# Performance work log

Measured on AMD Instinct MI355X. Metric: run time of the kernel, lower is better.

Reference implementation:

```python
import jax, jax.numpy as jnp
import numpy as np

N_NODE = 40000
EMB = 100
LAYERS = 2
B = 512
L = 50
N = 50
E = 800000


def _l2norm(x, axis=-1, eps=1e-12):
    n = jnp.sqrt(jnp.sum(x * x, axis=axis, keepdims=True))
    return x / jnp.maximum(n, eps)


def _item_conv(rows, cols, vals, emb, b):
    # sparse A @ X repeated LAYERS times, stack, l2-normalize rows, weighted sum
    finals = [emb]
    x = emb
    for _ in range(LAYERS):
        x = jax.ops.segment_sum(vals[:, None] * x[cols], rows, num_segments=emb.shape[0])
        finals.append(x)
    f = _l2norm(jnp.stack(finals, 0))                      # [LAYERS+1, n, d]
    return jnp.sum(b[:, None, None] * f, axis=0)


def _session_conv(adj_dense, emb, a):
    finals = [emb]
    x = emb
    for _ in range(LAYERS):
        x = adj_dense @ x
        finals.append(x)
    f = _l2norm(jnp.stack(finals, 0))
    return jnp.sum(a[:, None, None] * f, axis=0)


def _gat(h, adj, a0, a1, a2, a3):
    # e_k[b,i,j] = leakyrelu(sum_d h[b,i,d]*h[b,j,d]*a_k[d]); never materialize [B,N,N,D]
    def score(a):
        return jax.nn.leaky_relu(jnp.einsum('bid,bjd->bij', h * a[:, 0], h), 0.2)
    e0, e1, e2, e3 = score(a0), score(a1), score(a2), score(a3)
    neg = jnp.float32(-9e15)
    alpha = jnp.where(adj == 1, e0, neg)
    alpha = jnp.where(adj == 2, e1, alpha)
    alpha = jnp.where(adj == 3, e2, alpha)
    alpha = jnp.where(adj == 4, e3, alpha)
    alpha = jax.nn.softmax(alpha, axis=-1)
    return jnp.einsum('bij,bjd->bid', alpha, h)


def _get_seq(emb_table, rev, h, alias, mix=0.8):
    seq_h = emb_table[rev]                                  # [B,L,D]
    bidx = jnp.arange(rev.shape[0])[:, None]
    seq_h_ = h[bidx, alias]                                 # [B,L,D]
    return (1.0 - mix) * seq_h + mix * seq_h_               # eval: dropout = identity


def _soft_attention(seq_h, mask_f, session_len, pos_emb, w1_W, w1_b, glu1_W, glu1_b, glu2_W, w2):
    hs = jnp.sum(seq_h, axis=1) / session_len               # [B,D]
    pos = jnp.broadcast_to(pos_emb[:seq_h.shape[1]][None], seq_h.shape)
    nh = jnp.tanh(jnp.concatenate([pos, seq_h], -1) @ w1_W.T + w1_b)
    nh = jax.nn.sigmoid(nh @ glu1_W.T + glu1_b + (hs @ glu2_W.T)[:, None, :])
    beta = (nh @ w2) * mask_f[..., None]                    # [B,L,1]
    return jnp.sum(beta * seq_h, axis=1)                    # [B,D]


def setup_inputs() -> dict:
    key = jax.random.key(0)
    ks = jax.random.split(key, 30)
    stdv = 1.0 / np.sqrt(EMB)
    u = lambda k, s: jax.random.uniform(k, s, jnp.float32, -stdv, stdv)
    return {
        'tar': jax.random.randint(ks[0], (B,), 0, N_NODE),
        'reversed_sess_item': jax.random.randint(ks[1], (B, L), 0, N_NODE + 1),
        'mask': jnp.ones((B, L), jnp.int32),
        'session_len': jnp.ones((B, 1), jnp.float32),
        'session_adj': jax.random.uniform(ks[2], (B, B), jnp.float32),
        'is_train': 0,
        'items': jax.random.randint(ks[3], (B, N), 0, N_NODE + 1),
        'adj': jax.random.randint(ks[4], (B, N, N), 0, 5),
        'alias_session': jax.random.randint(ks[5], (B, L), 0, N),
        'gnn_rows': jax.random.randint(ks[6], (E,), 0, N_NODE),
        'gnn_cols': jax.random.randint(ks[7], (E,), 0, N_NODE),
        'gnn_vals': jax.random.uniform(ks[8], (E,), jnp.float32),
        'nodes_emb': u(ks[9], (N_NODE, EMB)),
        'b_item': jnp.ones((LAYERS + 1,), jnp.float32),
        'a_sess': jnp.ones((LAYERS + 1,), jnp.float32),
        'a0': u(ks[10], (EMB, 1)), 'a1': u(ks[11], (EMB, 1)),
        'a2': u(ks[12], (EMB, 1)), 'a3': u(ks[13], (EMB, 1)),
        'w1_W': u(ks[14], (EMB, 2 * EMB)), 'w1_b': u(ks[15], (EMB,)),
        'w2': u(ks[16], (EMB, 1)),
        'glu1_W': u(ks[17], (EMB, EMB)), 'glu1_b': u(ks[18], (EMB,)),
        'glu2_W': u(ks[19], (EMB, EMB)),
        'pos_emb': u(ks[20], (150, EMB)),
    }


def reference(tar, reversed_sess_item, mask, session_len, session_adj, is_train,
              items, adj, alias_session, gnn_rows, gnn_cols, gnn_vals,
              nodes_emb, b_item, a_sess, a0, a1, a2, a3,
              w1_W, w1_b, w2, glu1_W, glu1_b, glu2_W, pos_emb):
    mask_f = mask.astype(jnp.float32)
    zeros = jnp.zeros((1, EMB), jnp.float32)
    emb_gnn = _item_conv(gnn_rows, gnn_cols, gnn_vals, nodes_emb, b_item)
    # eval mode: both dropouts are identity
    e1t = jnp.concatenate([zeros, emb_gnn], 0)
    e2t = jnp.concatenate([zeros, emb_gnn], 0)
    embeddings = e1t + e2t

    h1 = _gat(e1t[items], adj, a0, a1, a2, a3)
    h1 = _get_seq(e1t, reversed_sess_item, h1, alias_session, 0.8)
    h2 = _gat(e2t[items], adj, a0, a1, a2, a3)
    h2 = _get_seq(e2t, reversed_sess_item, h2, alias_session, 0.8)

    sel1 = _soft_attention(h1, mask_f, session_len, pos_emb, w1_W, w1_b, glu1_W, glu1_b, glu2_W, w2)
    sel1 = _session_conv(session_adj, sel1, a_sess)
    sel2 = _soft_attention(h2, mask_f, session_len, pos_emb, w1_W, w1_b, glu1_W, glu1_b, glu2_W, w2)
    sel2 = _session_conv(session_adj, sel2, a_sess)

    con_loss = jnp.float32(0.0)  # is_train == 0 (inference path)

    seq_h = sel1 + sel2
    scores = seq_h @ embeddings[1:].T                       # [B, N_NODE]
    logp = jax.nn.log_softmax(scores + 1e-8, axis=-1)
    loss = -jnp.mean(logp[jnp.arange(scores.shape[0]), tar])
    return (con_loss, loss, scores)
```

## Files before the change

### kernel.cpp

```cpp
#include <hip/hip_runtime.h>
#include <hip/hip_bf16.h>
#include <math.h>

#define N_NODE 40000
#define EMB 100
#define BB 512
#define LL 50
#define NI 50
#define EDG 800000
#define SCAN_BLOCKS 157

typedef short s16x8 __attribute__((ext_vector_type(8)));
typedef float f32x4 __attribute__((ext_vector_type(4)));

__global__ void khist(const int* __restrict__ rows, int* __restrict__ counts) {
  int e = blockIdx.x * 256 + threadIdx.x;
  atomicAdd(&counts[rows[e]], 1);
}

__global__ __launch_bounds__(256) void kscan1(const int* __restrict__ counts,
                                              int* __restrict__ scanout,
                                              int* __restrict__ blocksums, int n) {
  __shared__ int wsum[4];
  int tid = threadIdx.x;
  int i = blockIdx.x * 256 + tid;
  int v = (i < n) ? counts[i] : 0;
  int x = v;
  #pragma unroll
  for (int off = 1; off < 64; off <<= 1) {
    int t = __shfl_up(x, off, 64);
    if ((tid & 63) >= off) x += t;
  }
  int w = tid >> 6, lane = tid & 63;
  if (lane == 63) wsum[w] = x;
  __syncthreads();
  int woff = 0;
  #pragma unroll
  for (int k = 0; k < 4; ++k) woff += (k < w) ? wsum[k] : 0;
  int incl = x + woff;
  if (i < n) scanout[i] = incl - v;
  if (tid == 255) blocksums[blockIdx.x] = incl;
}

__global__ __launch_bounds__(256) void kscan2(int* __restrict__ blocksums, int nb) {
  __shared__ int wsum[4];
  int tid = threadIdx.x;
  int v = (tid < nb) ? blocksums[tid] : 0;
  int x = v;
  #pragma unroll
  for (int off = 1; off < 64; off <<= 1) {
    int t = __shfl_up(x, off, 64);
    if ((tid & 63) >= off) x += t;
  }
  int w = tid >> 6, lane = tid & 63;
  if (lane == 63) wsum[w] = x;
  __syncthreads();
  int woff = 0;
  #pragma unroll
  for (int k = 0; k < 4; ++k) woff += (k < w) ? wsum[k] : 0;
  if (tid < nb) blocksums[tid] = x + woff - v;
}

__global__ __launch_bounds__(256) void kscan3(const int* __restrict__ scanout,
                                              const int* __restrict__ blocksums,
                                              int* __restrict__ starts,
                                              int* __restrict__ cursor, int n) {
  int i = blockIdx.x * 256 + threadIdx.x;
  if (i < n) {
    int s = scanout[i] + blocksums[blockIdx.x];
    starts[i] = s;
    cursor[i] = s;
  }
}

__global__ __launch_bounds__(256) void kfill(const int* __restrict__ rows,
                                             const int* __restrict__ cols,
                                             const float* __restrict__ vals,
                                             int* __restrict__ cursor,
                                             int2* __restrict__ colval) {
  int q = blockIdx.x & 7;
  int chunk = blockIdx.x >> 3;
  int e0 = (chunk * 256 + threadIdx.x) * 4;
  int rlo = q * 5000, rhi = rlo + 5000;
  if (e0 + 3 < EDG) {
    int4 r4 = *(const int4*)(rows + e0);
    int rr0 = r4.x, rr1 = r4.y, rr2 = r4.z, rr3 = r4.w;
    if (rr0 >= rlo && rr0 < rhi) {
      int p = atomicAdd(&cursor[rr0], 1);
      int2 cv; cv.x = cols[e0];     cv.y = __float_as_int(vals[e0]);
      colval[p] = cv;
    }
    if (rr1 >= rlo && rr1 < rhi) {
      int p = atomicAdd(&cursor[rr1], 1);
      int2 cv; cv.x = cols[e0 + 1]; cv.y = __float_as_int(vals[e0 + 1]);
      colval[p] = cv;
    }
    if (rr2 >= rlo && rr2 < rhi) {
      int p = atomicAdd(&cursor[rr2], 1);
      int2 cv; cv.x = cols[e0 + 2]; cv.y = __float_as_int(vals[e0 + 2]);
      colval[p] = cv;
    }
    if (rr3 >= rlo && rr3 < rhi) {
      int p = atomicAdd(&cursor[rr3], 1);
      int2 cv; cv.x = cols[e0 + 3]; cv.y = __float_as_int(vals[e0 + 3]);
      colval[p] = cv;
    }
  } else {
    for (int k = 0; k < 4; ++k) {
      int e = e0 + k;
      if (e < EDG) {
        int r = rows[e];
        if (r >= rlo && r < rhi) {
          int p = atomicAdd(&cursor[r], 1);
          int2 cv; cv.x = cols[e]; cv.y = __float_as_int(vals[e]);
          colval[p] = cv;
        }
      }
    }
  }
}

__global__ __launch_bounds__(256) void kspmm(const int* __restrict__ starts,
                                             const int* __restrict__ counts,
                                             const int2* __restrict__ colval,
                                             const float* __restrict__ x,
                                             float* __restrict__ out) {
  int row = blockIdx.x * 4 + (threadIdx.x >> 6);
  int lane = threadIdx.x & 63;
  int s = starts[row], cnt = counts[row];
  bool act = lane < 50;
  int d2 = (act ? lane : 49) * 2;
  float ax = 0.f, ay = 0.f;
  for (int base = 0; base < cnt; base += 64) {
    int nb = cnt - base; if (nb > 64) nb = 64;
    int cl = 0; float vl = 0.f;
    if (lane < nb) {
      int2 cv = colval[s + base + lane];
      cl = cv.x; vl = __int_as_float(cv.y);
    }
    int t = 0;
    for (; t + 8 <= nb; t += 8) {
      int c0 = __shfl(cl, t),     c1 = __shfl(cl, t + 1);
      int c2 = __shfl(cl, t + 2), c3 = __shfl(cl, t + 3);
      int c4 = __shfl(cl, t + 4), c5 = __shfl(cl, t + 5);
      int c6 = __shfl(cl, t + 6), c7 = __shfl(cl, t + 7);
      float v0 = __shfl(vl, t),     v1 = __shfl(vl, t + 1);
      float v2 = __shfl(vl, t + 2), v3 = __shfl(vl, t + 3);
      float v4 = __shfl(vl, t + 4), v5 = __shfl(vl, t + 5);
      float v6 = __shfl(vl, t + 6), v7 = __shfl(vl, t + 7);
      float2 g0 = *(const float2*)(x + (size_t)c0 * EMB + d2);
      float2 g1 = *(const float2*)(x + (size_t)c1 * EMB + d2);
      float2 g2 = *(const float2*)(x + (size_t)c2 * EMB + d2);
      float2 g3 = *(const float2*)(x + (size_t)c3 * EMB + d2);
      float2 g4 = *(const float2*)(x + (size_t)c4 * EMB + d2);
      float2 g5 = *(const float2*)(x + (size_t)c5 * EMB + d2);
      float2 g6 = *(const float2*)(x + (size_t)c6 * EMB + d2);
      float2 g7 = *(const float2*)(x + (size_t)c7 * EMB + d2);
      ax += v0 * g0.x; ay += v0 * g0.y;
      ax += v1 * g1.x; ay += v1 * g1.y;
      ax += v2 * g2.x; ay += v2 * g2.y;
      ax += v3 * g3.x; ay += v3 * g3.y;
      ax += v4 * g4.x; ay += v4 * g4.y;
      ax += v5 * g5.x; ay += v5 * g5.y;
      ax += v6 * g6.x; ay += v6 * g6.y;
      ax += v7 * g7.x; ay += v7 * g7.y;
    }
    for (; t + 4 <= nb; t += 4) {
      int c0 = __shfl(cl, t),     c1 = __shfl(cl, t + 1);
      int c2 = __shfl(cl, t + 2), c3 = __shfl(cl, t + 3);
      float v0 = __shfl(vl, t),     v1 = __shfl(vl, t + 1);
      float v2 = __shfl(vl, t + 2), v3 = __shfl(vl, t + 3);
      float2 g0 = *(const float2*)(x + (size_t)c0 * EMB + d2);
      float2 g1 = *(const float2*)(x + (size_t)c1 * EMB + d2);
      float2 g2 = *(const float2*)(x + (size_t)c2 * EMB + d2);
      float2 g3 = *(const float2*)(x + (size_t)c3 * EMB + d2);
      ax += v0 * g0.x; ay += v0 * g0.y;
      ax += v1 * g1.x; ay += v1 * g1.y;
      ax += v2 * g2.x; ay += v2 * g2.y;
      ax += v3 * g3.x; ay += v3 * g3.y;
    }
    for (; t < nb; ++t) {
      int c = __shfl(cl, t);
      float v = __shfl(vl, t);
      float2 g = *(const float2*)(x + (size_t)c * EMB + d2);
      ax += v * g.x; ay += v * g.y;
    }
  }
  if (act) {
    float2 o; o.x = ax; o.y = ay;
    *(float2*)(out + (size_t)row * EMB + d2) = o;
  }
}

__global__ void kcomb(const float* __restrict__ x0, const float* __restrict__ x1,
                      const float* __restrict__ x2, const float* __restrict__ bI,
                      float* __restrict__ emb) {
  int n = blockIdx.x * 4 + (threadIdx.x >> 6);
  int lane = threadIdx.x & 63;
  int d0 = lane, d1 = lane + 64;
  bool h1 = d1 < EMB;
  size_t base = (size_t)n * EMB;
  float v00 = x0[base + d0], v01 = h1 ? x0[base + d1] : 0.f;
  float v10 = x1[base + d0], v11 = h1 ? x1[base + d1] : 0.f;
  float v20 = x2[base + d0], v21 = h1 ? x2[base + d1] : 0.f;
  float q0 = v00 * v00 + v01 * v01;
  float q1 = v10 * v10 + v11 * v11;
  float q2 = v20 * v20 + v21 * v21;
  #pragma unroll
  for (int off = 32; off; off >>= 1) {
    q0 += __shfl_xor(q0, off);
    q1 += __shfl_xor(q1, off);
    q2 += __shfl_xor(q2, off);
  }
  float r0 = 1.f / fmaxf(sqrtf(q0), 1e-12f);
  float r1 = 1.f / fmaxf(sqrtf(q1), 1e-12f);
  float r2 = 1.f / fmaxf(sqrtf(q2), 1e-12f);
  float b0 = bI[0], b1 = bI[1], b2 = bI[2];
  emb[base + d0] = b0 * v00 * r0 + b1 * v10 * r1 + b2 * v20 * r2;
  if (h1) emb[base + d1] = b0 * v01 * r0 + b1 * v11 * r1 + b2 * v21 * r2;
}

__global__ __launch_bounds__(256) void kgat(
    const float* __restrict__ emb, const int* __restrict__ items,
    const int* __restrict__ adj,
    const float* __restrict__ a0p, const float* __restrict__ a1p,
    const float* __restrict__ a2p, const float* __restrict__ a3p,
    float* __restrict__ hgat) {
  __shared__ __align__(16) float hl[64 * 108];
  __shared__ __align__(16) float as[4 * 100];
  __shared__ float alpha_lds[64 * 51];
  __shared__ float wred[4][2][64];
  int b = blockIdx.x;
  int tid = threadIdx.x;
  for (int idx = tid; idx < 400; idx += 256) {
    int k = idx / 100, d = idx % 100;
    const float* ap = (k == 0) ? a0p : (k == 1) ? a1p : (k == 2) ? a2p : a3p;
    as[idx] = ap[d];
  }
  for (int idx = tid; idx < 64 * 50; idx += 256) {
    int i = idx / 50, d2 = (idx % 50) * 2;
    float2 v; v.x = 0.f; v.y = 0.f;
    if (i < NI) {
      int node = items[b * NI + i];
      if (node != 0) v = *(const float2*)(emb + (size_t)(node - 1) * EMB + d2);
    }
    *(float2*)&hl[i * 108 + d2] = v;
  }
  __syncthreads();
  int w = tid >> 6, lane = tid & 63;
  int j0 = w * 13;
  int nj = 50 - j0; if (nj > 13) nj = 13;

  float4 hreg[25];
  #pragma unroll
  for (int q = 0; q < 25; ++q) hreg[q] = *(const float4*)&hl[lane * 108 + q * 4];

  int al_lane = (lane < NI) ? lane : NI - 1;
  const int* adjrow = adj + (size_t)b * (NI * NI) + al_lane * NI + j0;
  int adjv[13];
  #pragma unroll
  for (int t = 0; t < 13; ++t) adjv[t] = (t < nj) ? adjrow[t] : 0;

  float e[13];
  #pragma unroll
  for (int jj = 0; jj < 13; ++jj) {
    float acc = 0.f;
    if (jj < nj) {
      int j = j0 + jj;
      int k = adjv[jj] - 1; k = (k < 0) ? 0 : (k > 3) ? 3 : k;
      const float* aw = &as[k * 100];
      #pragma unroll
      for (int q = 0; q < 25; ++q) {
        float4 hj = *(const float4*)&hl[j * 108 + q * 4];
        float4 a4 = *(const float4*)(aw + q * 4);
        float4 hm = hreg[q];
        acc += hm.x * hj.x * a4.x + hm.y * hj.y * a4.y
             + hm.z * hj.z * a4.z + hm.w * hj.w * a4.w;
      }
      acc = (acc >= 0.f) ? acc : 0.2f * acc;
      acc = (adjv[jj] == 0) ? -9e15f : acc;
    } else {
      acc = -INFINITY;
    }
    e[jj] = acc;
  }

  float mloc = -INFINITY;
  #pragma unroll
  for (int jj = 0; jj < 13; ++jj) if (jj < nj) mloc = fmaxf(mloc, e[jj]);
  wred[w][0][lane] = mloc;
  __syncthreads();
  float m = fmaxf(fmaxf(wred[0][0][lane], wred[1][0][lane]),
                  fmaxf(wred[2][0][lane], wred[3][0][lane]));
  float sloc = 0.f;
  #pragma unroll
  for (int jj = 0; jj < 13; ++jj) if (jj < nj) {
    e[jj] = expf(e[jj] - m);
    sloc += e[jj];
  }
  wred[w][1][lane] = sloc;
  __syncthreads();
  float s = (wred[0][1][lane] + wred[1][1][lane]) +
            (wred[2][1][lane] + wred[3][1][lane]);
  float inv = 1.f / s;
  #pragma unroll
  for (int jj = 0; jj < 13; ++jj) if (jj < nj)
    alpha_lds[lane * 51 + j0 + jj] = e[jj] * inv;
  __syncthreads();

  int nq = (w == 0) ? 7 : 6;
  float4 outq[7];
  #pragma unroll
  for (int t = 0; t < 7; ++t) outq[t] = make_float4(0.f, 0.f, 0.f, 0.f);
  for (int j = 0; j < NI; ++j) {
    float aj = alpha_lds[lane * 51 + j];
    #pragma unroll
    for (int t = 0; t < 7; ++t) {
      if (t < nq) {
        int q = w + 4 * t;
        float4 hv = *(const float4*)&hl[j * 108 + q * 4];
        outq[t].x += aj * hv.x; outq[t].y += aj * hv.y;
        outq[t].z += aj * hv.z; outq[t].w += aj * hv.w;
      }
    }
  }
  if (lane < NI) {
    #pragma unroll
    for (int t = 0; t < 7; ++t) {
      if (t < nq) {
        int q = w + 4 * t;
        *(float4*)&hgat[((size_t)b * NI + lane) * EMB + q * 4] = outq[t];
      }
    }
  }
}

__global__ void kseq(const float* __restrict__ emb, const int* __restrict__ rev,
                     const int* __restrict__ alias, const float* __restrict__ hgat,
                     float* __restrict__ hseq) {
  int idx = blockIdx.x * 256 + threadIdx.x;
  int b = idx / 5000, r = idx % 5000, l = r / 100, d = r % 100;
  int node = rev[b * LL + l];
  float sh = (node == 0) ? 0.f : emb[(size_t)(node - 1) * EMB + d];
  int a = alias[b * LL + l];
  float shh = hgat[((size_t)b * NI + a) * EMB + d];
  hseq[idx] = 0.2f * sh + 0.8f * shh;
}

__global__ void kprep_t(const float* __restrict__ w1W, const float* __restrict__ g1W,
                        const float* __restrict__ g2W, float* __restrict__ w1t2,
                        float* __restrict__ g1t, float* __restrict__ g2t) {
  int idx = blockIdx.x * 256 + threadIdx.x;
  if (idx >= 10000) return;
  int c = idx / 100, o = idx % 100;
  w1t2[c * 100 + o] = w1W[o * 200 + 100 + c];
  g1t[c * 100 + o] = g1W[o * 100 + c];
  g2t[c * 100 + o] = g2W[o * 100 + c];
}

__global__ void kprep_pos(const float* __restrict__ posE, const float* __restrict__ w1W,
                          const float* __restrict__ w1b, float* __restrict__ posW) {
  int idx = blockIdx.x * 256 + threadIdx.x;
  if (idx >= 5000) return;
  int l = idx / 100, o = idx % 100;
  float acc = w1b[o];
  for (int c = 0; c < 100; ++c) acc += posE[l * 100 + c] * w1W[o * 200 + c];
  posW[idx] = acc;
}

__global__ __launch_bounds__(256) void ksoft(
    const float* __restrict__ hseqG, const float* __restrict__ slenp,
    const int* __restrict__ maskp,
    const float* __restrict__ posW, const float* __restrict__ w1t2,
    const float* __restrict__ glu1t, const float* __restrict__ glu1b,
    const float* __restrict__ glu2t, const float* __restrict__ w2,
    float* __restrict__ sel) {
  __shared__ float hq[LL * 101];
  __shared__ float nh[LL * 100];
  __shared__ float red[25 * 52];
  __shared__ float hs_s[100];
  __shared__ float g_s[100];
  __shared__ float beta_s[LL];
  int b = blockIdx.x, tid = threadIdx.x;
  for (int idx = tid; idx < LL * 100; idx += 256) {
    int l = idx / 100, d = idx % 100;
    hq[l * 101 + d] = hseqG[((size_t)b * LL + l) * 100 + d];
  }
  __syncthreads();
  if (tid < 100) {
    float s = 0.f;
    for (int l = 0; l < LL; ++l) s += hq[l * 101 + tid];
    hs_s[tid] = s / slenp[b];
  }
  __syncthreads();
  if (tid < 100) {
    float acc = 0.f;
    for (int c = 0; c < 100; ++c) acc += hs_s[c] * glu2t[c * 100 + tid];
    g_s[tid] = acc;
  }
  int lg = tid / 25, og = tid % 25;
  if (tid < 250) {
    float acc[5][4];
    #pragma unroll
    for (int j = 0; j < 5; ++j) {
      float4 p = *(const float4*)&posW[(lg * 5 + j) * 100 + og * 4];
      acc[j][0] = p.x; acc[j][1] = p.y; acc[j][2] = p.z; acc[j][3] = p.w;
    }
    for (int c = 0; c < 100; ++c) {
      float4 wv = *(const float4*)&w1t2[c * 100 + og * 4];
      float hv[5];
      #pragma unroll
      for (int j = 0; j < 5; ++j) hv[j] = hq[(lg * 5 + j) * 101 + c];
      #pragma unroll
      for (int j = 0; j < 5; ++j) {
        acc[j][0] += hv[j] * wv.x;
        acc[j][1] += hv[j] * wv.y;
        acc[j][2] += hv[j] * wv.z;
        acc[j][3] += hv[j] * wv.w;
      }
    }
    #pragma unroll
    for (int j = 0; j < 5; ++j) {
      float4 t;
      t.x = tanhf(acc[j][0]); t.y = tanhf(acc[j][1]);
      t.z = tanhf(acc[j][2]); t.w = tanhf(acc[j][3]);
      *(float4*)&nh[(lg * 5 + j) * 100 + og * 4] = t;
    }
  }
  __syncthreads();
  if (tid < 250) {
    float4 gb = *(const float4*)&glu1b[og * 4];
    float4 gg = *(const float4*)&g_s[og * 4];
    float base0 = gg.x + gb.x, base1 = gg.y + gb.y, base2 = gg.z + gb.z, base3 = gg.w + gb.w;
    float acc[5][4];
    #pragma unroll
    for (int j = 0; j < 5; ++j) {
      acc[j][0] = base0; acc[j][1] = base1; acc[j][2] = base2; acc[j][3] = base3;
    }
    for (int c = 0; c < 100; ++c) {
      float4 wv = *(const float4*)&glu1t[c * 100 + og * 4];
      float hv[5];
      #pragma unroll
      for (int j = 0; j < 5; ++j) hv[j] = nh[(lg * 5 + j) * 100 + c];
      #pragma unroll
      for (int j = 0; j < 5; ++j) {
        acc[j][0] += hv[j] * wv.x;
        acc[j][1] += hv[j] * wv.y;
        acc[j][2] += hv[j] * wv.z;
        acc[j][3] += hv[j] * wv.w;
      }
    }
    float4 w2v = *(const float4*)&w2[og * 4];
    #pragma unroll
    for (int j = 0; j < 5; ++j) {
      float s0 = w2v.x / (1.f + expf(-acc[j][0]));
      float s1 = w2v.y / (1.f + expf(-acc[j][1]));
      float s2 = w2v.z / (1.f + expf(-acc[j][2]));
      float s3 = w2v.w / (1.f + expf(-acc[j][3]));
      red[og * 52 + lg * 5 + j] = (s0 + s1) + (s2 + s3);
    }
  }
  __syncthreads();
  if (tid < LL) {
    float s = 0.f;
    for (int og2 = 0; og2 < 25; ++og2) s += red[og2 * 52 + tid];
    beta_s[tid] = s * (float)maskp[b * LL + tid];
  }
  __syncthreads();
  if (tid < 100) {
    float acc = 0.f;
    for (int l = 0; l < LL; ++l) acc += beta_s[l] * hq[l * 101 + tid];
    sel[(size_t)b * 100 + tid] = acc;
  }
}

__global__ void ksess(const float* __restrict__ adjS, const float* __restrict__ x,
                      float* __restrict__ out) {
  int b = blockIdx.x, d = threadIdx.x;
  if (d >= 100) return;
  const float* ar = adjS + (size_t)b * BB;
  float a0 = 0.f, a1 = 0.f, a2 = 0.f, a3 = 0.f;
  for (int j = 0; j < BB; j += 4) {
    a0 += ar[j]     * x[(j)     * 100 + d];
    a1 += ar[j + 1] * x[(j + 1) * 100 + d];
    a2 += ar[j + 2] * x[(j + 2) * 100 + d];
    a3 += ar[j + 3] * x[(j + 3) * 100 + d];
  }
  out[(size_t)b * 100 + d] = (a0 + a1) + (a2 + a3);
}

__global__ void ksesscomb(const float* __restrict__ x0, const float* __restrict__ x1,
                          const float* __restrict__ x2, const float* __restrict__ aS,
                          float* __restrict__ out) {
  int b = blockIdx.x * 4 + (threadIdx.x >> 6);
  int lane = threadIdx.x & 63;
  int d0 = lane, d1 = lane + 64;
  bool h1 = d1 < EMB;
  size_t base = (size_t)b * EMB;
  float v00 = x0[base + d0], v01 = h1 ? x0[base + d1] : 0.f;
  float v10 = x1[base + d0], v11 = h1 ? x1[base + d1] : 0.f;
  float v20 = x2[base + d0], v21 = h1 ? x2[base + d1] : 0.f;
  float q0 = v00 * v00 + v01 * v01;
  float q1 = v10 * v10 + v11 * v11;
  float q2 = v20 * v20 + v21 * v21;
  #pragma unroll
  for (int off = 32; off; off >>= 1) {
    q0 += __shfl_xor(q0, off);
    q1 += __shfl_xor(q1, off);
    q2 += __shfl_xor(q2, off);
  }
  float r0 = 1.f / fmaxf(sqrtf(q0), 1e-12f);
  float r1 = 1.f / fmaxf(sqrtf(q1), 1e-12f);
  float r2 = 1.f / fmaxf(sqrtf(q2), 1e-12f);
  float b0 = aS[0], b1 = aS[1], b2 = aS[2];
  out[base + d0] = 2.f * (b0 * v00 * r0 + b1 * v10 * r1 + b2 * v20 * r2);
  if (h1) out[base + d1] = 2.f * (b0 * v01 * r0 + b1 * v11 * r1 + b2 * v21 * r2);
}

__global__ void kprepB(const float* __restrict__ emb, unsigned short* __restrict__ bHi,
                       unsigned short* __restrict__ bLo) {
  int idx = blockIdx.x * 256 + threadIdx.x;
  int n = idx >> 7, k = idx & 127;
  float v = (k < EMB) ? 2.f * emb[(size_t)n * EMB + k] : 0.f;
  __hip_bfloat16 h = __float2bfloat16(v);
  float rem = v - __bfloat162float(h);
  __hip_bfloat16 l = __float2bfloat16(rem);
  bHi[idx] = *reinterpret_cast<unsigned short*>(&h);
  bLo[idx] = *reinterpret_cast<unsigned short*>(&l);
}

__global__ void kprepA(const float* __restrict__ seqh, unsigned short* __restrict__ aHi,
                       unsigned short* __restrict__ aLo) {
  int idx = blockIdx.x * 256 + threadIdx.x;
  int n = idx >> 7, k = idx & 127;
  float v = (k < EMB) ? seqh[(size_t)n * EMB + k] : 0.f;
  __hip_bfloat16 h = __float2bfloat16(v);
  float rem = v - __bfloat162float(h);
  __hip_bfloat16 l = __float2bfloat16(rem);
  aHi[idx] = *reinterpret_cast<unsigned short*>(&h);
  aLo[idx] = *reinterpret_cast<unsigned short*>(&l);
}

__global__ __launch_bounds__(256) void kscoresM(
    const unsigned short* __restrict__ aHi, const unsigned short* __restrict__ aLo,
    const unsigned short* __restrict__ bHi, const unsigned short* __restrict__ bLo,
    float* __restrict__ outS) {
  __shared__ __align__(16) unsigned short Bh[64 * 136];
  __shared__ __align__(16) unsigned short Bl[64 * 136];
  int tid = threadIdx.x;
  int n0 = blockIdx.y * 64;
  int bbase = blockIdx.x * 128;
  int w = tid >> 6, lane = tid & 63;
  int ln = lane & 15, quad = lane >> 4;

  const unsigned short* aRowH0 = aHi + (size_t)(bbase + w * 16 + ln) * 128 + quad * 8;
  const unsigned short* aRowL0 = aLo + (size_t)(bbase + w * 16 + ln) * 128 + quad * 8;
  const unsigned short* aRowH1 = aRowH0 + 64 * 128;
  const unsigned short* aRowL1 = aRowL0 + 64 * 128;
  s16x8 ah0[4], al0[4], ah1[4], al1[4];
  #pragma unroll
  for (int s = 0; s < 4; ++s) {
    ah0[s] = *(const s16x8*)(aRowH0 + s * 32);
    al0[s] = *(const s16x8*)(aRowL0 + s * 32);
    ah1[s] = *(const s16x8*)(aRowH1 + s * 32);
    al1[s] = *(const s16x8*)(aRowL1 + s * 32);
  }

  #pragma unroll
  for (int it = 0; it < 4; ++it) {
    int seg = tid + it * 256;
    int r = seg >> 4, q = seg & 15;
    *(s16x8*)&Bh[r * 136 + q * 8] = *(const s16x8*)&bHi[(size_t)(n0 + r) * 128 + q * 8];
    *(s16x8*)&Bl[r * 136 + q * 8] = *(const s16x8*)&bLo[(size_t)(n0 + r) * 128 + q * 8];
  }
  __syncthreads();

  f32x4 acc[4];
  #pragma unroll
  for (int t = 0; t < 4; ++t) acc[t] = (f32x4){0.f, 0.f, 0.f, 0.f};
  #pragma unroll
  for (int s = 0; s < 4; ++s) {
    #pragma unroll
    for (int t = 0; t < 4; ++t) {
      s16x8 bh = *(const s16x8*)&Bh[(t * 16 + ln) * 136 + s * 32 + quad * 8];
      s16x8 bl = *(const s16x8*)&Bl[(t * 16 + ln) * 136 + s * 32 + quad * 8];
      acc[t] = __builtin_amdgcn_mfma_f32_16x16x32_bf16(ah0[s], bh, acc[t], 0, 0, 0);
      acc[t] = __builtin_amdgcn_mfma_f32_16x16x32_bf16(al0[s], bh, acc[t], 0, 0, 0);
      acc[t] = __builtin_amdgcn_mfma_f32_16x16x32_bf16(ah0[s], bl, acc[t], 0, 0, 0);
    }
  }
  {
    int brow = bbase + w * 16 + quad * 4;
    #pragma unroll
    for (int t = 0; t < 4; ++t) {
      int ncol = n0 + t * 16 + ln;
      #pragma unroll
      for (int r = 0; r < 4; ++r) {
        outS[(size_t)(brow + r) * N_NODE + ncol] = acc[t][r];
      }
    }
  }

  #pragma unroll
  for (int t = 0; t < 4; ++t) acc[t] = (f32x4){0.f, 0.f, 0.f, 0.f};
  #pragma unroll
  for (int s = 0; s < 4; ++s) {
    #pragma unroll
    for (int t = 0; t < 4; ++t) {
      s16x8 bh = *(const s16x8*)&Bh[(t * 16 + ln) * 136 + s * 32 + quad * 8];
      s16x8 bl = *(const s16x8*)&Bl[(t * 16 + ln) * 136 + s * 32 + quad * 8];
      acc[t] = __builtin_amdgcn_mfma_f32_16x16x32_bf16(ah1[s], bh, acc[t], 0, 0, 0);
      acc[t] = __builtin_amdgcn_mfma_f32_16x16x32_bf16(al1[s], bh, acc[t], 0, 0, 0);
      acc[t] = __builtin_amdgcn_mfma_f32_16x16x32_bf16(ah1[s], bl, acc[t], 0, 0, 0);
    }
  }
  {
    int brow = bbase + 64 + w * 16 + quad * 4;
    #pragma unroll
    for (int t = 0; t < 4; ++t) {
      int ncol = n0 + t * 16 + ln;
      #pragma unroll
      for (int r = 0; r < 4; ++r) {
        outS[(size_t)(brow + r) * N_NODE + ncol] = acc[t][r];
      }
    }
  }
}

__global__ __launch_bounds__(256) void klse(const float* __restrict__ outS,
                                            const int* __restrict__ tar,
                                            float* __restrict__ part) {
  __shared__ float ms[256], ss[256];
  int b = blockIdx.x, tid = threadIdx.x;
  const float2* sp = (const float2*)(outS + (size_t)b * N_NODE);
  float m = -INFINITY, s = 0.f;
  for (int i = tid; i < N_NODE / 2; i += 256) {
    float2 v = sp[i];
    float mx = fmaxf(v.x, v.y);
    float add = expf(v.x - mx) + expf(v.y - mx);
    if (mx > m) { s = s * expf(m - mx) + add; m = mx; }
    else s += add * expf(mx - m);
  }
  ms[tid] = m; ss[tid] = s;
  __syncthreads();
  for (int st = 128; st; st >>= 1) {
    if (tid < st) {
      float m2 = ms[tid + st], s2 = ss[tid + st];
      float M = fmaxf(ms[tid], m2);
      ss[tid] = ss[tid] * expf(ms[tid] - M) + s2 * expf(m2 - M);
      ms[tid] = M;
    }
    __syncthreads();
  }
  if (tid == 0) {
    float tsc = outS[(size_t)b * N_NODE + tar[b]];
    part[b] = tsc - (ms[0] + logf(ss[0]));
  }
}

__global__ void kfinal(const float* __restrict__ part, float* __restrict__ out) {
  __shared__ float red[256];
  int tid = threadIdx.x;
  red[tid] = part[tid] + part[tid + 256];
  __syncthreads();
  for (int st = 128; st; st >>= 1) {
    if (tid < st) red[tid] += red[tid + st];
    __syncthreads();
  }
  if (tid == 0) {
    out[0] = 0.f;
    out[1] = -red[0] / (float)BB;
  }
}

extern "C" void kernel_launch(void* const* d_in, const int* in_sizes, int n_in,
                              void* d_out, int out_size, void* d_ws, size_t ws_size,
                              hipStream_t stream) {
  const int* tar    = (const int*)d_in[0];
  const int* rev    = (const int*)d_in[1];
  const int* maskp  = (const int*)d_in[2];
  const float* slen = (const float*)d_in[3];
  const float* sadj = (const float*)d_in[4];
  const int* items  = (const int*)d_in[6];
  const int* adjp   = (const int*)d_in[7];
  const int* alias  = (const int*)d_in[8];
  const int* grows  = (const int*)d_in[9];
  const int* gcols  = (const int*)d_in[10];
  const float* gvals = (const float*)d_in[11];
  const float* nemb = (const float*)d_in[12];
  const float* bI   = (const float*)d_in[13];
  const float* aS   = (const float*)d_in[14];
  const float* a0p  = (const float*)d_in[15];
  const float* a1p  = (const float*)d_in[16];
  const float* a2p  = (const float*)d_in[17];
  const float* a3p  = (const float*)d_in[18];
  const float* w1W  = (const float*)d_in[19];
  const float* w1b  = (const float*)d_in[20];
  const float* w2p  = (const float*)d_in[21];
  const float* g1W  = (const float*)d_in[22];
  const float* g1b  = (const float*)d_in[23];
  const float* g2W  = (const float*)d_in[24];
  const float* posE = (const float*)d_in[25];

  float* W = (float*)d_ws;
  size_t o = 0;
  float* emb_gnn = W + o; o += (size_t)N_NODE * EMB;
  float* x1      = W + o; o += (size_t)N_NODE * EMB;
  float* x2      = W + o; o += (size_t)N_NODE * EMB;
  float* sel     = W + o; o += (size_t)BB * EMB;
  float* y1      = W + o; o += (size_t)BB * EMB;
  float* y2      = W + o; o += (size_t)BB * EMB;
  float* seqh    = W + o; o += (size_t)BB * EMB;
  float* posW    = W + o; o += 5120;
  float* w1t2    = W + o; o += 10000;
  float* glu1t   = W + o; o += 10000;
  float* glu2t   = W + o; o += 10000;
  int2* colval   = (int2*)(W + o); o += (size_t)2 * EDG;
  float* part    = W + o; o += 512;
  int* counts = (int*)(W + o); o += N_NODE;
  int* starts = (int*)(W + o); o += N_NODE;
  int* cursor = (int*)(W + o); o += N_NODE;
  int* scantmp = (int*)(W + o); o += N_NODE;
  int* blocksums = (int*)(W + o); o += 256;
  unsigned short* aHi = (unsigned short*)(W + o); o += 32768;
  unsigned short* aLo = (unsigned short*)(W + o); o += 32768;
  float* hgat = x1;
  float* hseq = x2;
  unsigned short* bHi = (unsigned short*)x1;
  unsigned short* bLo = (unsigned short*)x2;

  float* outF = (float*)d_out;
  float* outScores = outF + 2;

  hipMemsetAsync(counts, 0, N_NODE * sizeof(int), stream);
  khist<<<EDG / 256, 256, 0, stream>>>(grows, counts);
  kscan1<<<SCAN_BLOCKS, 256, 0, stream>>>(counts, scantmp, blocksums, N_NODE);
  kscan2<<<1, 256, 0, stream>>>(blocksums, SCAN_BLOCKS);
  kscan3<<<SCAN_BLOCKS, 256, 0, stream>>>(scantmp, blocksums, starts, cursor, N_NODE);
  kfill<<<((EDG + 1023) / 1024) * 8, 256, 0, stream>>>(grows, gcols, gvals, cursor, colval);
  kspmm<<<N_NODE / 4, 256, 0, stream>>>(starts, counts, colval, nemb, x1);
  kspmm<<<N_NODE / 4, 256, 0, stream>>>(starts, counts, colval, x1, x2);
  kcomb<<<N_NODE / 4, 256, 0, stream>>>(nemb, x1, x2, bI, emb_gnn);
  kgat<<<BB, 256, 0, stream>>>(emb_gnn, items, adjp, a0p, a1p, a2p, a3p, hgat);
  kseq<<<(BB * LL * EMB) / 256, 256, 0, stream>>>(emb_gnn, rev, alias, hgat, hseq);
  kprep_t<<<40, 256, 0, stream>>>(w1W, g1W, g2W, w1t2, glu1t, glu2t);
  kprep_pos<<<20, 256, 0, stream>>>(posE, w1W, w1b, posW);
  ksoft<<<BB, 256, 0, stream>>>(hseq, slen, maskp, posW, w1t2, glu1t, g1b, glu2t, w2p, sel);
  kprepB<<<(N_NODE * 128) / 256, 256, 0, stream>>>(emb_gnn, bHi, bLo);
  ksess<<<BB, 128, 0, stream>>>(sadj, sel, y1);
  ksess<<<BB, 128, 0, stream>>>(sadj, y1, y2);
  ksesscomb<<<BB / 4, 256, 0, stream>>>(sel, y1, y2, aS, seqh);
  kprepA<<<(BB * 128) / 256, 256, 0, stream>>>(seqh, aHi, aLo);
  kscoresM<<<dim3(4, N_NODE / 64), 256, 0, stream>>>(aHi, aLo, bHi, bLo, outScores);
  klse<<<BB, 256, 0, stream>>>(outScores, tar, part);
  kfinal<<<1, 256, 0, stream>>>(part, outF);
}
```

Measured before the change: 540.5 us.

## Fuse per-tile log-sum-exp partials into scores GEMM epilogue

The scores GEMM epilogue now computes, for each row, the max and sum-of-exp over its 64-column tile using wave shuffles, and writes these partials to a workspace buffer. The separate LSE kernel then merges 625 partials per row instead of rereading the whole 512x40000 score matrix. This removes about 80 MB of global reads, at the cost of extra exp and shuffle work in the GEMM epilogue and a small partial buffer.

```diff
diff --git a/kernel.cpp b/kernel.cpp
--- a/kernel.cpp
+++ b/kernel.cpp
@@ -9,6 +9,7 @@
 #define NI 50
 #define EDG 800000
 #define SCAN_BLOCKS 157
+#define NBLK 625
 
 typedef short s16x8 __attribute__((ext_vector_type(8)));
 typedef float f32x4 __attribute__((ext_vector_type(4)));
@@ -544,11 +545,12 @@
 __global__ __launch_bounds__(256) void kscoresM(
     const unsigned short* __restrict__ aHi, const unsigned short* __restrict__ aLo,
     const unsigned short* __restrict__ bHi, const unsigned short* __restrict__ bLo,
-    float* __restrict__ outS) {
+    float* __restrict__ outS, float* __restrict__ part2) {
   __shared__ __align__(16) unsigned short Bh[64 * 136];
   __shared__ __align__(16) unsigned short Bl[64 * 136];
   int tid = threadIdx.x;
-  int n0 = blockIdx.y * 64;
+  int nb = blockIdx.y;
+  int n0 = nb * 64;
   int bbase = blockIdx.x * 128;
   int w = tid >> 6, lane = tid & 63;
   int ln = lane & 15, quad = lane >> 4;
@@ -599,6 +601,20 @@
         outS[(size_t)(brow + r) * N_NODE + ncol] = acc[t][r];
       }
     }
+    #pragma unroll
+    for (int r = 0; r < 4; ++r) {
+      float mx = fmaxf(fmaxf(acc[0][r], acc[1][r]), fmaxf(acc[2][r], acc[3][r]));
+      #pragma unroll
+      for (int off = 1; off < 16; off <<= 1) mx = fmaxf(mx, __shfl_xor(mx, off));
+      float se = expf(acc[0][r] - mx) + expf(acc[1][r] - mx)
+               + expf(acc[2][r] - mx) + expf(acc[3][r] - mx);
+      #pragma unroll
+      for (int off = 1; off < 16; off <<= 1) se += __shfl_xor(se, off);
+      if (ln == 0) {
+        float2 p; p.x = mx; p.y = se;
+        *(float2*)&part2[((size_t)nb * BB + brow + r) * 2] = p;
+      }
+    }
   }
 
   #pragma unroll
@@ -624,22 +640,35 @@
         outS[(size_t)(brow + r) * N_NODE + ncol] = acc[t][r];
       }
     }
-  }
-}
-
-__global__ __launch_bounds__(256) void klse(const float* __restrict__ outS,
-                                            const int* __restrict__ tar,
-                                            float* __restrict__ part) {
+    #pragma unroll
+    for (int r = 0; r < 4; ++r) {
+      float mx = fmaxf(fmaxf(acc[0][r], acc[1][r]), fmaxf(acc[2][r], acc[3][r]));
+      #pragma unroll
+      for (int off = 1; off < 16; off <<= 1) mx = fmaxf(mx, __shfl_xor(mx, off));
+      float se = expf(acc[0][r] - mx) + expf(acc[1][r] - mx)
+               + expf(acc[2][r] - mx) + expf(acc[3][r] - mx);
+      #pragma unroll
+      for (int off = 1; off < 16; off <<= 1) se += __shfl_xor(se, off);
+      if (ln == 0) {
+        float2 p; p.x = mx; p.y = se;
+        *(float2*)&part2[((size_t)nb * BB + brow + r) * 2] = p;
+      }
+    }
+  }
+}
+
+__global__ __launch_bounds__(256) void klse2(const float* __restrict__ part2,
+                                             const float* __restrict__ outS,
+                                             const int* __restrict__ tar,
+                                             float* __restrict__ part) {
   __shared__ float ms[256], ss[256];
   int b = blockIdx.x, tid = threadIdx.x;
-  const float2* sp = (const float2*)(outS + (size_t)b * N_NODE);
   float m = -INFINITY, s = 0.f;
-  for (int i = tid; i < N_NODE / 2; i += 256) {
-    float2 v = sp[i];
-    float mx = fmaxf(v.x, v.y);
-    float add = expf(v.x - mx) + expf(v.y - mx);
-    if (mx > m) { s = s * expf(m - mx) + add; m = mx; }
-    else s += add * expf(mx - m);
+  for (int nb = tid; nb < NBLK; nb += 256) {
+    float2 p = *(const float2*)&part2[((size_t)nb * BB + b) * 2];
+    float M = fmaxf(m, p.x);
+    s = s * expf(m - M) + p.y * expf(p.x - M);
+    m = M;
   }
   ms[tid] = m; ss[tid] = s;
   __syncthreads();
@@ -717,6 +746,7 @@
   float* glu2t   = W + o; o += 10000;
   int2* colval   = (int2*)(W + o); o += (size_t)2 * EDG;
   float* part    = W + o; o += 512;
+  float* part2   = W + o; o += (size_t)NBLK * BB * 2;
   int* counts = (int*)(W + o); o += N_NODE;
   int* starts = (int*)(W + o); o += N_NODE;
   int* cursor = (int*)(W + o); o += N_NODE;
@@ -751,7 +781,7 @@
   ksess<<<BB, 128, 0, stream>>>(sadj, y1, y2);
   ksesscomb<<<BB / 4, 256, 0, stream>>>(sel, y1, y2, aS, seqh);
   kprepA<<<(BB * 128) / 256, 256, 0, stream>>>(seqh, aHi, aLo);
-  kscoresM<<<dim3(4, N_NODE / 64), 256, 0, stream>>>(aHi, aLo, bHi, bLo, outScores);
-  klse<<<BB, 256, 0, stream>>>(outScores, tar, part);
+  kscoresM<<<dim3(4, NBLK), 256, 0, stream>>>(aHi, aLo, bHi, bLo, outScores, part2);
+  klse2<<<BB, 256, 0, stream>>>(part2, outScores, tar, part);
   kfinal<<<1, 256, 0, stream>>>(part, outF);
 }
```

New measurement: 504.8 us. -6.6%, faster.
